# Performance work log

Hardware: AMD Instinct MI355X
Metric: run time of the kernel (lower is better)

## Reference

```python
import jax, jax.numpy as jnp
import numpy as np

NUM_HEADS = 16
NUM_KV_HEADS = 4
HEAD_DIM = 128
EPS = 1e-6


def _rotate_half(x):
    x1, x2 = jnp.split(x, 2, axis=-1)
    return jnp.concatenate((-x2, x1), axis=-1)


def _rms_norm(x, w):
    var = jnp.mean(x * x, axis=-1, keepdims=True)
    return x * jax.lax.rsqrt(var + EPS) * w


def setup_inputs() -> dict:
    key = jax.random.key(0)
    ks = jax.random.split(key, 6)
    B, S, H = 2, 2048, 2048
    hidden_states = jax.random.normal(ks[0], (B, S, H), dtype=jnp.float32)
    # real RoPE tables (HF-style: freqs tiled twice along last dim)
    inv_freq = 1.0 / (10000.0 ** (np.arange(0, HEAD_DIM, 2, dtype=np.float32) / HEAD_DIM))
    pos = np.arange(S, dtype=np.float32)
    ang = np.concatenate([pos[:, None] * inv_freq[None, :]] * 2, axis=-1)  # [S, head_dim]
    cos = jnp.broadcast_to(jnp.cos(ang)[None], (B, S, HEAD_DIM)).astype(jnp.float32)
    sin = jnp.broadcast_to(jnp.sin(ang)[None], (B, S, HEAD_DIM)).astype(jnp.float32)
    sc = 0.02
    Wq = jax.random.normal(ks[1], (NUM_HEADS * HEAD_DIM, H), dtype=jnp.float32) * sc
    Wk = jax.random.normal(ks[2], (NUM_KV_HEADS * HEAD_DIM, H), dtype=jnp.float32) * sc
    Wv = jax.random.normal(ks[3], (NUM_KV_HEADS * HEAD_DIM, H), dtype=jnp.float32) * sc
    Wo = jax.random.normal(ks[4], (H, NUM_HEADS * HEAD_DIM), dtype=jnp.float32) * sc
    q_norm_w = jnp.ones((HEAD_DIM,), dtype=jnp.float32)
    k_norm_w = jnp.ones((HEAD_DIM,), dtype=jnp.float32)
    return {"hidden_states": hidden_states, "cos": cos, "sin": sin,
            "Wq": Wq, "Wk": Wk, "Wv": Wv, "Wo": Wo,
            "q_norm_w": q_norm_w, "k_norm_w": k_norm_w}


def reference(hidden_states, cos, sin, Wq, Wk, Wv, Wo, q_norm_w, k_norm_w):
    B, S, H = hidden_states.shape
    groups = NUM_HEADS // NUM_KV_HEADS
    # projections (Linear: x @ W^T), then [B, h, S, d]
    q = (hidden_states @ Wq.T).reshape(B, S, NUM_HEADS, HEAD_DIM).transpose(0, 2, 1, 3)
    k = (hidden_states @ Wk.T).reshape(B, S, NUM_KV_HEADS, HEAD_DIM).transpose(0, 2, 1, 3)
    v = (hidden_states @ Wv.T).reshape(B, S, NUM_KV_HEADS, HEAD_DIM).transpose(0, 2, 1, 3)
    # per-head RMSNorm
    q = _rms_norm(q, q_norm_w)
    k = _rms_norm(k, k_norm_w)
    # RoPE, cos/sin broadcast over heads (unsqueeze_dim=1)
    c = cos[:, None, :, :]
    s = sin[:, None, :, :]
    q = q * c + _rotate_half(q) * s
    k = k * c + _rotate_half(k) * s
    # GQA: expand kv heads
    k = jnp.repeat(k, groups, axis=1)
    v = jnp.repeat(v, groups, axis=1)
    scale = 1.0 / jnp.sqrt(jnp.float32(HEAD_DIM))
    scores = jnp.einsum('bhqd,bhkd->bhqk', q, k) * scale
    attn = jax.nn.softmax(scores, axis=-1)
    out = jnp.einsum('bhqk,bhkd->bhqd', attn, v)
    out = out.transpose(0, 2, 1, 3).reshape(B, S, NUM_HEADS * HEAD_DIM)
    return out @ Wo.T
```

## Files before the change

### kernel.cpp

```cpp
#include <hip/hip_runtime.h>
#include <hip/hip_bf16.h>
#include <stdint.h>

typedef __attribute__((ext_vector_type(8))) short short8;
typedef __attribute__((ext_vector_type(4))) float floatx4;
typedef __attribute__((ext_vector_type(16))) float floatx16;

#define MFMA16(a, b, c) __builtin_amdgcn_mfma_f32_16x16x32_bf16(a, b, c, 0, 0, 0)
#define MFMA32(a, b, c) __builtin_amdgcn_mfma_f32_32x32x16_bf16(a, b, c, 0, 0, 0)

static __device__ __forceinline__ void gload_lds16(const __hip_bfloat16* g, __hip_bfloat16* l) {
  __builtin_amdgcn_global_load_lds(
      (const __attribute__((address_space(1))) void*)g,
      (__attribute__((address_space(3))) void*)l,
      16, 0, 0);
}

__global__ void f2bf(const float* __restrict__ in, __hip_bfloat16* __restrict__ out, int n) {
  const int stride = gridDim.x * blockDim.x * 4;
  for (int i = (blockIdx.x * blockDim.x + threadIdx.x) * 4; i < n; i += stride) {
    const float4 v = *(const float4*)(in + i);
    __hip_bfloat16 t[4] = {__float2bfloat16(v.x), __float2bfloat16(v.y),
                           __float2bfloat16(v.z), __float2bfloat16(v.w)};
    *(short4*)(out + i) = *(const short4*)t;
  }
}

template <typename OUT_T>
__global__ __launch_bounds__(256)
void gemm_bt(const __hip_bfloat16* __restrict__ A, const __hip_bfloat16* __restrict__ Bt,
             OUT_T* __restrict__ C, int M, int N, int K) {
  __shared__ __hip_bfloat16 As[2][128 * 32];
  __shared__ __hip_bfloat16 Bs[2][128 * 32];
  const int tid = threadIdx.x;
  const int wid = tid >> 6, lane = tid & 63;
  const int lg = lane >> 4, lr = lane & 15;
  const int wr = wid >> 1, wc = wid & 1;
  const int m0 = blockIdx.x * 128, n0 = blockIdx.y * 128;
  const int nk = K >> 5;

  floatx4 acc[4][4];
#pragma unroll
  for (int mi = 0; mi < 4; ++mi)
#pragma unroll
    for (int ni = 0; ni < 4; ++ni) acc[mi][ni] = (floatx4)(0.0f);

  auto stage = [&](int buf, int kt) {
    const int k0 = kt << 5;
#pragma unroll
    for (int i = 0; i < 2; ++i) {
      const int e = (i * 256 + tid) * 8;
      const int row = e >> 5, col = e & 31;
      gload_lds16(A + (size_t)(m0 + row) * K + k0 + col, &As[buf][e]);
    }
#pragma unroll
    for (int i = 0; i < 2; ++i) {
      const int e = (i * 256 + tid) * 8;
      const int row = e >> 5, col = e & 31;
      gload_lds16(Bt + (size_t)(n0 + row) * K + k0 + col, &Bs[buf][e]);
    }
  };

  stage(0, 0);
  __syncthreads();

  for (int kt = 0; kt < nk; ++kt) {
    const int cur = kt & 1;
    if (kt + 1 < nk) stage(cur ^ 1, kt + 1);
    short8 af[4], bfr[4];
#pragma unroll
    for (int mi = 0; mi < 4; ++mi)
      af[mi] = *(const short8*)&As[cur][(wr * 64 + mi * 16 + lr) * 32 + lg * 8];
#pragma unroll
    for (int ni = 0; ni < 4; ++ni)
      bfr[ni] = *(const short8*)&Bs[cur][(wc * 64 + ni * 16 + lr) * 32 + lg * 8];
#pragma unroll
    for (int mi = 0; mi < 4; ++mi)
#pragma unroll
      for (int ni = 0; ni < 4; ++ni) acc[mi][ni] = MFMA16(af[mi], bfr[ni], acc[mi][ni]);
    __syncthreads();
  }

#pragma unroll
  for (int mi = 0; mi < 4; ++mi)
#pragma unroll
    for (int ni = 0; ni < 4; ++ni) {
      const int row = m0 + wr * 64 + mi * 16 + lg * 4;
      const int col = n0 + wc * 64 + ni * 16 + lr;
#pragma unroll
      for (int r = 0; r < 4; ++r) {
        C[(size_t)(row + r) * N + col] = (OUT_T)acc[mi][ni][r];
      }
    }
}

__global__ __launch_bounds__(256)
void normrope(const __hip_bfloat16* __restrict__ qkv, const float* __restrict__ cosb,
              const float* __restrict__ sinb, const float* __restrict__ qw,
              const float* __restrict__ kw, __hip_bfloat16* __restrict__ Q,
              __hip_bfloat16* __restrict__ K) {
  const int m = blockIdx.x;
  const int b = m >> 11, s = m & 2047;
  const int wid = threadIdx.x >> 6, lane = threadIdx.x & 63;
  const size_t qkvrow = (size_t)m * 3072;
  const float c1 = cosb[(size_t)m * 128 + lane], s1 = sinb[(size_t)m * 128 + lane];
  const float c2 = cosb[(size_t)m * 128 + lane + 64], s2 = sinb[(size_t)m * 128 + lane + 64];
  for (int h = wid * 5; h < wid * 5 + 5; ++h) {
    const float x1 = __bfloat162float(qkv[qkvrow + h * 128 + lane]);
    const float x2 = __bfloat162float(qkv[qkvrow + h * 128 + lane + 64]);
    float ss = x1 * x1 + x2 * x2;
    ss += __shfl_xor(ss, 1);  ss += __shfl_xor(ss, 2);  ss += __shfl_xor(ss, 4);
    ss += __shfl_xor(ss, 8);  ss += __shfl_xor(ss, 16); ss += __shfl_xor(ss, 32);
    const float rs = rsqrtf(ss * (1.0f / 128.0f) + 1e-6f);
    const float* w = (h < 16) ? qw : kw;
    const float n1 = x1 * rs * w[lane], n2 = x2 * rs * w[lane + 64];
    const float o1 = n1 * c1 - n2 * s1;
    const float o2 = n2 * c2 + n1 * s2;
    if (h < 16) {
      const size_t base = ((size_t)(b * 16 + h) * 2048 + s) * 128;
      Q[base + lane] = __float2bfloat16(o1);
      Q[base + lane + 64] = __float2bfloat16(o2);
    } else {
      const size_t base = ((size_t)(b * 4 + h - 16) * 2048 + s) * 128;
      K[base + lane] = __float2bfloat16(o1);
      K[base + lane + 64] = __float2bfloat16(o2);
    }
  }
}

__global__ __launch_bounds__(256)
void kblock(const __hip_bfloat16* __restrict__ K, __hip_bfloat16* __restrict__ Kb2) {
  const int z = blockIdx.y;
  const int t = blockIdx.x * 4 + (threadIdx.x >> 6);
  const int kv = threadIdx.x & 63;
  const short* src = (const short*)K + (size_t)z * 262144 + t * 8192;
  short* dst = (short*)Kb2 + (size_t)z * 262144 + t * 8192;
#pragma unroll
  for (int cd = 0; cd < 16; ++cd) {
    const short8 v = *(const short8*)&src[kv * 128 + cd * 8];
    *(short8*)&dst[cd * 512 + kv * 8] = v;
  }
}

__global__ __launch_bounds__(256)
void vtrans2(const __hip_bfloat16* __restrict__ qkv, __hip_bfloat16* __restrict__ Vt2) {
  __shared__ short L[64 * 65];
  const int tid = threadIdx.x;
  const int t = blockIdx.x, d0 = blockIdx.y * 64, z = blockIdx.z;
  const int b = z >> 2, hkv = z & 3;
  const int s0 = t * 64;
#pragma unroll
  for (int i = 0; i < 2; ++i) {
    const int slot = i * 256 + tid;
    const int srow = slot >> 3, c8 = (slot & 7) * 8;
    const short8 v = *(const short8*)((const short*)qkv +
        (size_t)(b * 2048 + s0 + srow) * 3072 + 2560 + hkv * 128 + d0 + c8);
#pragma unroll
    for (int j = 0; j < 8; ++j) L[(c8 + j) * 65 + srow] = v[j];
  }
  __syncthreads();
  short* dst = (short*)Vt2 + (size_t)z * 262144 + t * 8192;
#pragma unroll
  for (int i = 0; i < 2; ++i) {
    const int slot = i * 256 + tid;
    const int drow = slot >> 3, sc8 = (slot & 7) * 8;
    short8 o;
#pragma unroll
    for (int j = 0; j < 8; ++j) {
      const int p = sc8 + j;
      const int pb = p & 31;
      const int phys = (p & ~31) | ((pb & 3) + ((pb >> 2) & 1) * 8 + ((pb >> 3) & 1) * 4 + (pb & 16));
      o[j] = L[drow * 65 + phys];
    }
    *(short8*)&dst[(sc8 >> 3) * 1024 + (d0 + drow) * 8] = o;
  }
}

__global__ __launch_bounds__(256, 2)
void fattn(const __hip_bfloat16* __restrict__ Qg, const __hip_bfloat16* __restrict__ Kb2,
           const __hip_bfloat16* __restrict__ Vt2, __hip_bfloat16* __restrict__ Og) {
  __shared__ short SMEM[2][16384];

  const int tid = threadIdx.x, wid = tid >> 6, lane = tid & 63;
  const int l31 = lane & 31, hi = lane >> 5;
  const int qt = blockIdx.x, bh = blockIdx.y;
  const int b = bh >> 4, h = bh & 15, hkv = h >> 2;
  const int z = b * 4 + hkv;
  const int q0w = qt * 128 + wid * 32;

  const __hip_bfloat16* Qrow = Qg + ((size_t)((b * 16 + h) * 2048 + q0w + l31)) * 128;
  short8 qf2[8];
#pragma unroll
  for (int ks = 0; ks < 8; ++ks) qf2[ks] = *(const short8*)(Qrow + ks * 16 + hi * 8);

  const short* Kbase = (const short*)Kb2 + (size_t)z * 262144;
  const short* Vbase = (const short*)Vt2 + (size_t)z * 262144;

  auto stage = [&](int buf, int t) {
    const short* ks = Kbase + t * 8192 + wid * 2048 + lane * 8;
    const short* vs = Vbase + t * 8192 + wid * 2048 + lane * 8;
    short* kd = &SMEM[buf][wid * 2048];
    short* vd = &SMEM[buf][8192 + wid * 2048];
#pragma unroll
    for (int i = 0; i < 4; ++i)
      gload_lds16((const __hip_bfloat16*)(ks + i * 512), (__hip_bfloat16*)(kd + i * 512));
#pragma unroll
    for (int i = 0; i < 4; ++i)
      gload_lds16((const __hip_bfloat16*)(vs + i * 512), (__hip_bfloat16*)(vd + i * 512));
  };

  floatx16 oacc[4];
#pragma unroll
  for (int dblk = 0; dblk < 4; ++dblk) oacc[dblk] = (floatx16)(0.0f);
  float la0 = 0.0f, la1 = 0.0f;

  const float SC2 = 0.12753102497113446f;
  const float OFF2 = 17.31234049066756f;

  stage(0, 0);
  asm volatile("s_waitcnt vmcnt(0)" ::: "memory");
  __builtin_amdgcn_s_barrier();
  __builtin_amdgcn_sched_barrier(0);

  for (int t = 0; t < 32; ++t) {
    const int cur = t & 1;
    const short* Kt = SMEM[cur];
    const short* Vt = SMEM[cur] + 8192;
    if (t + 1 < 32) stage(cur ^ 1, t + 1);

    floatx16 st[2];
    st[0] = (floatx16)(0.0f);
    st[1] = (floatx16)(0.0f);
    __builtin_amdgcn_s_setprio(1);
#pragma unroll
    for (int ks = 0; ks < 8; ++ks) {
      const short8 kf0 = *(const short8*)&Kt[(ks * 2 + hi) * 512 + l31 * 8];
      const short8 kf1 = *(const short8*)&Kt[(ks * 2 + hi) * 512 + 256 + l31 * 8];
      st[0] = MFMA32(kf0, qf2[ks], st[0]);
      st[1] = MFMA32(kf1, qf2[ks], st[1]);
    }
    __builtin_amdgcn_s_setprio(0);

    int pk[2][8];
#pragma unroll
    for (int kvblk = 0; kvblk < 2; ++kvblk)
#pragma unroll
      for (int m = 0; m < 8; ++m) {
        const float e0 = exp2f(fmaf(st[kvblk][2 * m], SC2, -OFF2));
        const float e1 = exp2f(fmaf(st[kvblk][2 * m + 1], SC2, -OFF2));
        if (m & 1) la1 += e0 + e1; else la0 += e0 + e1;
        asm("v_cvt_pk_bf16_f32 %0, %1, %2" : "=v"(pk[kvblk][m]) : "v"(e0), "v"(e1));
      }

#pragma unroll
    for (int kvblk = 0; kvblk < 2; ++kvblk) {
#pragma unroll
      for (int s = 0; s < 2; ++s) {
        union { int i[4]; short8 s8; } u;
        u.i[0] = pk[kvblk][4 * s + 0];
        u.i[1] = pk[kvblk][4 * s + 1];
        u.i[2] = pk[kvblk][4 * s + 2];
        u.i[3] = pk[kvblk][4 * s + 3];
        const short8 pB = u.s8;
        const int c = kvblk * 4 + s * 2 + hi;
        __builtin_amdgcn_s_setprio(1);
#pragma unroll
        for (int dblk = 0; dblk < 4; ++dblk) {
          const short8 vf = *(const short8*)&Vt[c * 1024 + dblk * 256 + l31 * 8];
          oacc[dblk] = MFMA32(vf, pB, oacc[dblk]);
        }
        __builtin_amdgcn_s_setprio(0);
      }
    }

    asm volatile("s_waitcnt vmcnt(0)" ::: "memory");
    __builtin_amdgcn_s_barrier();
    __builtin_amdgcn_sched_barrier(0);
  }

  const float l_own = la0 + la1;
  const float l = l_own + __shfl_xor(l_own, 32);
  const float inv = 1.0f / l;
  short* tw = &SMEM[0][0] + wid * 4352;
#pragma unroll
  for (int dblk = 0; dblk < 4; ++dblk)
#pragma unroll
    for (int a = 0; a < 4; ++a) {
      __hip_bfloat16 o4[4];
#pragma unroll
      for (int r = 0; r < 4; ++r) o4[r] = __float2bfloat16(oacc[dblk][4 * a + r] * inv);
      *(short4*)&tw[l31 * 136 + dblk * 32 + a * 8 + hi * 4] = *(const short4*)o4;
    }
  __hip_bfloat16* orow =
      Og + ((size_t)(b * 2048 + q0w + (lane >> 1))) * 2048 + h * 128 + (lane & 1) * 64;
  const short* trow = &tw[(lane >> 1) * 136 + (lane & 1) * 64];
#pragma unroll
  for (int c = 0; c < 8; ++c) {
    *(short8*)(orow + c * 8) = *(const short8*)(trow + c * 8);
  }
}

extern "C" void kernel_launch(void* const* d_in, const int* in_sizes, int n_in,
                              void* d_out, int out_size, void* d_ws, size_t ws_size,
                              hipStream_t stream) {
  const float* hidden = (const float*)d_in[0];
  const float* cosb = (const float*)d_in[1];
  const float* sinb = (const float*)d_in[2];
  const float* Wq = (const float*)d_in[3];
  const float* Wk = (const float*)d_in[4];
  const float* Wv = (const float*)d_in[5];
  const float* Wo = (const float*)d_in[6];
  const float* qw = (const float*)d_in[7];
  const float* kw = (const float*)d_in[8];

  char* ws = (char*)d_ws;
  __hip_bfloat16* hidden_bf = (__hip_bfloat16*)ws; ws += (size_t)4096 * 2048 * 2;
  __hip_bfloat16* wqkv = (__hip_bfloat16*)ws;      ws += (size_t)3072 * 2048 * 2;
  __hip_bfloat16* wo_bf = (__hip_bfloat16*)ws;     ws += (size_t)2048 * 2048 * 2;
  __hip_bfloat16* qkv = (__hip_bfloat16*)ws;       ws += (size_t)4096 * 3072 * 2;
  __hip_bfloat16* Qb = (__hip_bfloat16*)ws;        ws += (size_t)2 * 16 * 2048 * 128 * 2;
  __hip_bfloat16* Kb = (__hip_bfloat16*)ws;        ws += (size_t)2 * 4 * 2048 * 128 * 2;
  __hip_bfloat16* Kb2 = (__hip_bfloat16*)ws;       ws += (size_t)2 * 4 * 2048 * 128 * 2;
  __hip_bfloat16* attn = (__hip_bfloat16*)ws;      ws += (size_t)4096 * 2048 * 2;
  __hip_bfloat16* Vt2 = wqkv;

  f2bf<<<1024, 256, 0, stream>>>(hidden, hidden_bf, 4096 * 2048);
  f2bf<<<1024, 256, 0, stream>>>(Wq, wqkv, 2048 * 2048);
  f2bf<<<512, 256, 0, stream>>>(Wk, wqkv + (size_t)2048 * 2048, 512 * 2048);
  f2bf<<<512, 256, 0, stream>>>(Wv, wqkv + (size_t)2560 * 2048, 512 * 2048);
  f2bf<<<1024, 256, 0, stream>>>(Wo, wo_bf, 2048 * 2048);

  gemm_bt<__hip_bfloat16><<<dim3(32, 24), 256, 0, stream>>>(hidden_bf, wqkv, qkv, 4096, 3072, 2048);
  normrope<<<4096, 256, 0, stream>>>(qkv, cosb, sinb, qw, kw, Qb, Kb);
  kblock<<<dim3(8, 8), 256, 0, stream>>>(Kb, Kb2);
  vtrans2<<<dim3(32, 2, 8), 256, 0, stream>>>(qkv, Vt2);
  fattn<<<dim3(16, 32), 256, 0, stream>>>(Qb, Kb2, Vt2, attn);
  gemm_bt<float><<<dim3(32, 16), 256, 0, stream>>>(attn, wo_bf, (float*)d_out, 4096, 2048, 2048);
}
```

Measured before the change: 244.0 us.

## Software-pipeline attention PV with QK/exp and fuse fp32-to-bf16 conversions

Restructures the flash-attention loop so the P·V MFMAs for the previous KV tile are issued alongside the Q·K MFMAs and exponentials of the current tile. V gets a triple-buffered LDS slot ring and K stays double-buffered, raising shared memory to 80KB per block. Separately, the five fp32-to-bf16 conversion launches are merged into one kernel with block-range dispatch. The risks are higher register pressure from two live probability arrays and the larger LDS footprint, which could cut occupancy.

```diff
diff --git a/kernel.cpp b/kernel.cpp
--- a/kernel.cpp
+++ b/kernel.cpp
@@ -16,14 +16,25 @@
       16, 0, 0);
 }
 
-__global__ void f2bf(const float* __restrict__ in, __hip_bfloat16* __restrict__ out, int n) {
-  const int stride = gridDim.x * blockDim.x * 4;
-  for (int i = (blockIdx.x * blockDim.x + threadIdx.x) * 4; i < n; i += stride) {
-    const float4 v = *(const float4*)(in + i);
-    __hip_bfloat16 t[4] = {__float2bfloat16(v.x), __float2bfloat16(v.y),
-                           __float2bfloat16(v.z), __float2bfloat16(v.w)};
-    *(short4*)(out + i) = *(const short4*)t;
-  }
+__global__ __launch_bounds__(256)
+void f2bf_all(const float* __restrict__ h, const float* __restrict__ wq,
+              const float* __restrict__ wk, const float* __restrict__ wv,
+              const float* __restrict__ wo, __hip_bfloat16* __restrict__ hb,
+              __hip_bfloat16* __restrict__ wqkv, __hip_bfloat16* __restrict__ wob) {
+  const int blk = blockIdx.x;
+  const float* src;
+  __hip_bfloat16* dst;
+  int off;
+  if (blk < 8192)       { src = h;  dst = hb;                          off = blk; }
+  else if (blk < 12288) { src = wq; dst = wqkv;                        off = blk - 8192; }
+  else if (blk < 13312) { src = wk; dst = wqkv + (size_t)2048 * 2048;  off = blk - 12288; }
+  else if (blk < 14336) { src = wv; dst = wqkv + (size_t)2560 * 2048;  off = blk - 13312; }
+  else                  { src = wo; dst = wob;                         off = blk - 14336; }
+  const int i = off * 1024 + threadIdx.x * 4;
+  const float4 v = *(const float4*)(src + i);
+  __hip_bfloat16 t[4] = {__float2bfloat16(v.x), __float2bfloat16(v.y),
+                         __float2bfloat16(v.z), __float2bfloat16(v.w)};
+  *(short4*)(dst + i) = *(const short4*)t;
 }
 
 template <typename OUT_T>
@@ -179,7 +190,7 @@
 __global__ __launch_bounds__(256, 2)
 void fattn(const __hip_bfloat16* __restrict__ Qg, const __hip_bfloat16* __restrict__ Kb2,
            const __hip_bfloat16* __restrict__ Vt2, __hip_bfloat16* __restrict__ Og) {
-  __shared__ short SMEM[2][16384];
+  __shared__ short SMEM[40960];
 
   const int tid = threadIdx.x, wid = tid >> 6, lane = tid & 63;
   const int l31 = lane & 31, hi = lane >> 5;
@@ -196,14 +207,16 @@
   const short* Kbase = (const short*)Kb2 + (size_t)z * 262144;
   const short* Vbase = (const short*)Vt2 + (size_t)z * 262144;
 
-  auto stage = [&](int buf, int t) {
+  auto stageK = [&](int buf, int t) {
     const short* ks = Kbase + t * 8192 + wid * 2048 + lane * 8;
-    const short* vs = Vbase + t * 8192 + wid * 2048 + lane * 8;
-    short* kd = &SMEM[buf][wid * 2048];
-    short* vd = &SMEM[buf][8192 + wid * 2048];
+    short* kd = &SMEM[buf * 8192 + wid * 2048];
 #pragma unroll
     for (int i = 0; i < 4; ++i)
       gload_lds16((const __hip_bfloat16*)(ks + i * 512), (__hip_bfloat16*)(kd + i * 512));
+  };
+  auto stageV = [&](int slot, int t) {
+    const short* vs = Vbase + t * 8192 + wid * 2048 + lane * 8;
+    short* vd = &SMEM[16384 + slot * 8192 + wid * 2048];
 #pragma unroll
     for (int i = 0; i < 4; ++i)
       gload_lds16((const __hip_bfloat16*)(vs + i * 512), (__hip_bfloat16*)(vd + i * 512));
@@ -217,18 +230,10 @@
   const float SC2 = 0.12753102497113446f;
   const float OFF2 = 17.31234049066756f;
 
-  stage(0, 0);
-  asm volatile("s_waitcnt vmcnt(0)" ::: "memory");
-  __builtin_amdgcn_s_barrier();
-  __builtin_amdgcn_sched_barrier(0);
-
-  for (int t = 0; t < 32; ++t) {
-    const int cur = t & 1;
-    const short* Kt = SMEM[cur];
-    const short* Vt = SMEM[cur] + 8192;
-    if (t + 1 < 32) stage(cur ^ 1, t + 1);
-
-    floatx16 st[2];
+  int pkA[2][8], pkB[2][8];
+
+  auto doQK = [&](int kbuf, floatx16 (&st)[2]) {
+    const short* Kt = &SMEM[kbuf * 8192];
     st[0] = (floatx16)(0.0f);
     st[1] = (floatx16)(0.0f);
     __builtin_amdgcn_s_setprio(1);
@@ -240,8 +245,8 @@
       st[1] = MFMA32(kf1, qf2[ks], st[1]);
     }
     __builtin_amdgcn_s_setprio(0);
-
-    int pk[2][8];
+  };
+  auto doExp = [&](const floatx16 (&st)[2], int (&pk)[2][8]) {
 #pragma unroll
     for (int kvblk = 0; kvblk < 2; ++kvblk)
 #pragma unroll
@@ -251,7 +256,9 @@
         if (m & 1) la1 += e0 + e1; else la0 += e0 + e1;
         asm("v_cvt_pk_bf16_f32 %0, %1, %2" : "=v"(pk[kvblk][m]) : "v"(e0), "v"(e1));
       }
-
+  };
+  auto doPV = [&](int vslot, const int (&pk)[2][8]) {
+    const short* Vt = &SMEM[16384 + vslot * 8192];
 #pragma unroll
     for (int kvblk = 0; kvblk < 2; ++kvblk) {
 #pragma unroll
@@ -272,16 +279,52 @@
         __builtin_amdgcn_s_setprio(0);
       }
     }
-
+  };
+
+  int vs_stage = 2, vs_pv = 0;
+  auto body = [&](int (&pkPrev)[2][8], int (&pkCur)[2][8], int u) {
+    if (u + 1 < 32) {
+      stageK((u + 1) & 1, u + 1);
+      stageV(vs_stage, u + 1);
+    }
+    floatx16 st[2];
+    doQK(u & 1, st);
+    doPV(vs_pv, pkPrev);
+    doExp(st, pkCur);
+    vs_stage = (vs_stage == 2) ? 0 : vs_stage + 1;
+    vs_pv = (vs_pv == 2) ? 0 : vs_pv + 1;
     asm volatile("s_waitcnt vmcnt(0)" ::: "memory");
     __builtin_amdgcn_s_barrier();
     __builtin_amdgcn_sched_barrier(0);
-  }
+  };
+
+  stageK(0, 0);
+  stageV(0, 0);
+  asm volatile("s_waitcnt vmcnt(0)" ::: "memory");
+  __builtin_amdgcn_s_barrier();
+  __builtin_amdgcn_sched_barrier(0);
+  {
+    stageK(1, 1);
+    stageV(1, 1);
+    floatx16 st[2];
+    doQK(0, st);
+    doExp(st, pkA);
+    asm volatile("s_waitcnt vmcnt(0)" ::: "memory");
+    __builtin_amdgcn_s_barrier();
+    __builtin_amdgcn_sched_barrier(0);
+  }
+
+  for (int u = 1; u < 31; u += 2) {
+    body(pkA, pkB, u);
+    body(pkB, pkA, u + 1);
+  }
+  body(pkA, pkB, 31);
+  doPV(vs_pv, pkB);
 
   const float l_own = la0 + la1;
   const float l = l_own + __shfl_xor(l_own, 32);
   const float inv = 1.0f / l;
-  short* tw = &SMEM[0][0] + wid * 4352;
+  short* tw = &SMEM[wid * 4352];
 #pragma unroll
   for (int dblk = 0; dblk < 4; ++dblk)
 #pragma unroll
@@ -324,11 +367,7 @@
   __hip_bfloat16* attn = (__hip_bfloat16*)ws;      ws += (size_t)4096 * 2048 * 2;
   __hip_bfloat16* Vt2 = wqkv;
 
-  f2bf<<<1024, 256, 0, stream>>>(hidden, hidden_bf, 4096 * 2048);
-  f2bf<<<1024, 256, 0, stream>>>(Wq, wqkv, 2048 * 2048);
-  f2bf<<<512, 256, 0, stream>>>(Wk, wqkv + (size_t)2048 * 2048, 512 * 2048);
-  f2bf<<<512, 256, 0, stream>>>(Wv, wqkv + (size_t)2560 * 2048, 512 * 2048);
-  f2bf<<<1024, 256, 0, stream>>>(Wo, wo_bf, 2048 * 2048);
+  f2bf_all<<<18432, 256, 0, stream>>>(hidden, Wq, Wk, Wv, Wo, hidden_bf, wqkv, wo_bf);
 
   gemm_bt<__hip_bfloat16><<<dim3(32, 24), 256, 0, stream>>>(hidden_bf, wqkv, qkv, 4096, 3072, 2048);
   normrope<<<4096, 256, 0, stream>>>(qkv, cosb, sinb, qw, kw, Qb, Kb);
```

Result: faster. 234.7 us (-3.8%).
